# Kernel optimization log

Measured on AMD Instinct MI355X. Metric: run time of the kernel, lower is better.

The kernel has to match this reference:

```python
import jax, jax.numpy as jnp
import numpy as np

H = 512   # d_model (hidden)
L = 2     # rnn_layer_dim
E = 321   # enc_in
C = 321   # c_out (must equal enc_in: decoder output is fed back as input)
T = 96    # seq_len
P = 96    # pred_len
B = 512   # batch


def _cell(x, h, c, Wih, Whh, bih, bhh):
    # PyTorch LSTM gate order: input, forget, cell(g), output
    g = x @ Wih.T + h @ Whh.T + bih + bhh
    i, f, gg, o = jnp.split(g, 4, axis=-1)
    c = jax.nn.sigmoid(f) * c + jax.nn.sigmoid(i) * jnp.tanh(gg)
    h = jax.nn.sigmoid(o) * jnp.tanh(c)
    return h, c


def _run_layer(xs, Wih, Whh, bih, bhh):
    # xs: [T, B, in_dim] -> ys: [T, B, H], final (h, c)
    b = xs.shape[1]
    h0 = jnp.zeros((b, Whh.shape[1]), xs.dtype)
    def step(carry, x):
        h, c = carry
        h, c = _cell(x, h, c, Wih, Whh, bih, bhh)
        return (h, c), h
    (h, c), ys = jax.lax.scan(step, (h0, h0), xs)
    return ys, h, c


def _forward(x_enc, x_mark_enc, x_dec, x_mark_dec,
             e_Wih0, e_Whh0, e_bih0, e_bhh0, e_Wih1, e_Whh1, e_bih1, e_bhh1,
             d_Wih0, d_Whh0, d_bih0, d_bhh0, d_Wih1, d_Whh1, d_bih1, d_bhh1,
             fc_W, fc_b):
    del x_mark_enc, x_dec, x_mark_dec  # unused in use_tf=False path
    xs = jnp.swapaxes(x_enc, 0, 1)                     # [T, B, E]
    ys, h0, c0 = _run_layer(xs, e_Wih0, e_Whh0, e_bih0, e_bhh0)
    _,  h1, c1 = _run_layer(ys, e_Wih1, e_Whh1, e_bih1, e_bhh1)

    inp0 = x_enc[:, -1, :]                             # [B, E] last source step

    def dec_step(carry, _):
        inp, h0, c0, h1, c1 = carry
        h0, c0 = _cell(inp, h0, c0, d_Wih0, d_Whh0, d_bih0, d_bhh0)
        h1, c1 = _cell(h0,  h1, c1, d_Wih1, d_Whh1, d_bih1, d_bhh1)
        out = h1 @ fc_W.T + fc_b                       # [B, C]
        return (out, h0, c0, h1, c1), out

    _, outs = jax.lax.scan(dec_step, (inp0, h0, c0, h1, c1), None, length=P)
    return jnp.swapaxes(outs, 0, 1)                    # [B, P, C]


def setup_inputs() -> dict:
    key = jax.random.key(0)
    ks = jax.random.split(key, 24)
    s = 1.0 / np.sqrt(H)  # PyTorch LSTM init scale
    def w(k, shape):
        return jax.random.uniform(k, shape, jnp.float32, -s, s)
    inp = {
        "x_enc": jax.random.normal(ks[0], (B, T, E), jnp.float32),
        "x_mark_enc": jax.random.normal(ks[1], (B, T, 4), jnp.float32),
        "x_dec": jax.random.normal(ks[2], (B, P, C), jnp.float32),
        "x_mark_dec": jax.random.normal(ks[3], (B, P, 4), jnp.float32),
        "e_Wih0": w(ks[4], (4 * H, E)),  "e_Whh0": w(ks[5], (4 * H, H)),
        "e_bih0": w(ks[6], (4 * H,)),    "e_bhh0": w(ks[7], (4 * H,)),
        "e_Wih1": w(ks[8], (4 * H, H)),  "e_Whh1": w(ks[9], (4 * H, H)),
        "e_bih1": w(ks[10], (4 * H,)),   "e_bhh1": w(ks[11], (4 * H,)),
        "d_Wih0": w(ks[12], (4 * H, E)), "d_Whh0": w(ks[13], (4 * H, H)),
        "d_bih0": w(ks[14], (4 * H,)),   "d_bhh0": w(ks[15], (4 * H,)),
        "d_Wih1": w(ks[16], (4 * H, H)), "d_Whh1": w(ks[17], (4 * H, H)),
        "d_bih1": w(ks[18], (4 * H,)),   "d_bhh1": w(ks[19], (4 * H,)),
        "fc_W": w(ks[20], (C, H)),       "fc_b": w(ks[21], (C,)),
    }
    return inp


def reference(x_enc, x_mark_enc, x_dec, x_mark_dec,
              e_Wih0, e_Whh0, e_bih0, e_bhh0, e_Wih1, e_Whh1, e_bih1, e_bhh1,
              d_Wih0, d_Whh0, d_bih0, d_bhh0, d_Wih1, d_Whh1, d_bih1, d_bhh1,
              fc_W, fc_b):
    return _forward(x_enc, x_mark_enc, x_dec, x_mark_dec,
                    e_Wih0, e_Whh0, e_bih0, e_bhh0, e_Wih1, e_Whh1, e_bih1, e_bhh1,
                    d_Wih0, d_Whh0, d_bih0, d_bhh0, d_Wih1, d_Whh1, d_bih1, d_bhh1,
                    fc_W, fc_b)
```

## Files before the change

kernel.cpp:

```cpp
#include <hip/hip_runtime.h>
#include <hip/hip_bf16.h>

#define BB 512
#define TT 96
#define PP 96
#define EE 321
#define CC 321
#define HH 512
#define G4 2048
#define EPAD 352
#define NFC 384

#define BUF_SZ 24576
#define XH_OFF 0
#define XL_OFF 8192
#define WH_OFF 16384
#define WL_OFF 20480
#define FC_SMEM 49152

#define LSTM_SMEM 81920

typedef unsigned short u16;
typedef __attribute__((ext_vector_type(8))) short bf16x8;
typedef __attribute__((ext_vector_type(16))) float floatx16;

__device__ __forceinline__ void splitf(float v, u16& h, u16& l){
  __hip_bfloat16 bh = __float2bfloat16(v);
  h = *reinterpret_cast<u16*>(&bh);
  float r = v - __bfloat162float(bh);
  __hip_bfloat16 bl = __float2bfloat16(r);
  l = *reinterpret_cast<u16*>(&bl);
}

__device__ __forceinline__ void gload16(const void* g, void* l){
  __builtin_amdgcn_global_load_lds((const __attribute__((address_space(1))) void*)g,
                                   (__attribute__((address_space(3))) void*)l, 16, 0, 0);
}

struct SJob { const float* src; u16* hi; u16* lo; int rows, cols, rowspad, colspad; };
struct SJobs { SJob j[9]; };

__global__ void split_multi(SJobs js){
  const int stride = gridDim.x * blockDim.x;
  const int t0 = blockIdx.x * blockDim.x + threadIdx.x;
  for (int k = 0; k < 9; ++k){
    const SJob J = js.j[k];
    const int total = J.rowspad * J.colspad;
    for (int idx = t0; idx < total; idx += stride){
      int r = idx / J.colspad, cc = idx - r * J.colspad;
      float v = (r < J.rows && cc < J.cols) ? J.src[(size_t)r * J.cols + cc] : 0.f;
      u16 h, l; splitf(v, h, l);
      J.hi[idx] = h; J.lo[idx] = l;
    }
  }
}

__global__ void wcomb_fused(const float* __restrict__ A,
                            const float* __restrict__ Bm,
                            const float* __restrict__ bih, const float* __restrict__ bhh,
                            const float* __restrict__ fcb,
                            u16* __restrict__ Wc_h, u16* __restrict__ Wc_l,
                            float* __restrict__ bd0c){
  __shared__ float arow[EE];
  __shared__ float red[256];
  const int g = blockIdx.x;
  for (int e = threadIdx.x; e < EE; e += 256) arow[e] = A[(size_t)g * EE + e];
  __syncthreads();
  float ps = 0.f;
  for (int e = threadIdx.x; e < EE; e += 256) ps += arow[e] * fcb[e];
  red[threadIdx.x] = ps; __syncthreads();
  for (int s = 128; s > 0; s >>= 1){
    if (threadIdx.x < s) red[threadIdx.x] += red[threadIdx.x + s];
    __syncthreads();
  }
  if (threadIdx.x == 0) bd0c[g] = bih[g] + bhh[g] + red[0];
  for (int k = threadIdx.x; k < HH; k += 256){
    float s = 0.f;
    for (int e = 0; e < EE; ++e) s += arow[e] * Bm[(size_t)e * HH + k];
    u16 h, l; splitf(s, h, l);
    Wc_h[(size_t)g * HH + k] = h; Wc_l[(size_t)g * HH + k] = l;
  }
}

__global__ void prep_misc(
    const float* e_bih0, const float* e_bhh0, float* be0,
    const float* e_bih1, const float* e_bhh1, float* be1,
    const float* d_bih0, const float* d_bhh0, float* bd0,
    const float* d_bih1, const float* d_bhh1, float* bd1,
    const float* fc_b, float* bfc,
    const float* x_enc, u16* inph, u16* inpl, u16* xh, u16* xl){
  const int stride = gridDim.x * blockDim.x;
  const int t0 = blockIdx.x * blockDim.x + threadIdx.x;
  for (int i = t0; i < G4; i += stride){
    be0[i] = e_bih0[i] + e_bhh0[i];
    be1[i] = e_bih1[i] + e_bhh1[i];
    bd0[i] = d_bih0[i] + d_bhh0[i];
    bd1[i] = d_bih1[i] + d_bhh1[i];
  }
  for (int i = t0; i < NFC; i += stride) bfc[i] = (i < CC) ? fc_b[i] : 0.f;
  for (int idx = t0; idx < BB * EPAD; idx += stride){
    int b = idx / EPAD, j = idx - b * EPAD;
    float v = (j < EE) ? x_enc[(size_t)b * TT * EE + (size_t)(TT - 1) * EE + j] : 0.f;
    u16 h, l; splitf(v, h, l);
    inph[idx] = h; inpl[idx] = l;
  }
  for (int idx = t0; idx < TT * BB * EPAD; idx += stride){
    int e = idx % EPAD;
    int rest = idx / EPAD;
    int b = rest % BB;
    int t = rest / BB;
    float v = (e < EE) ? x_enc[((size_t)b * TT + t) * EE + e] : 0.f;
    u16 h, l; splitf(v, h, l);
    xh[idx] = h; xl[idx] = l;
  }
}

template<int MT>
__device__ __forceinline__ void lstm_body(
    char* smem, int bx,
    const u16* __restrict__ Xh, const u16* __restrict__ Xl, int K1pad,
    const u16* __restrict__ Wih_h, const u16* __restrict__ Wih_l,
    const u16* __restrict__ Whh_h, const u16* __restrict__ Whh_l,
    const float* __restrict__ bias, const float* __restrict__ Gin,
    const u16* __restrict__ Hph, const u16* __restrict__ Hpl,
    u16* __restrict__ Hnh, u16* __restrict__ Hnl,
    float* __restrict__ cst)
{
  constexpr int XROWB = MT * 64;
  constexpr int BUFB  = 2 * XROWB + 8192;
  constexpr int WH_O  = 2 * XROWB;
  constexpr int WL_O  = 2 * XROWB + 4096;

  float (*sG)[68] = (float (*)[68])(smem);

  const int tid  = threadIdx.x;
  const int lane = tid & 63;
  const int wid  = tid >> 6;
  const int wm = wid >> 1, wn = wid & 1;
  const int m0 = (bx >> 5) * MT;
  const int u0 = (bx & 31) * 16;

  floatx16 acc0 = {0.f,0.f,0.f,0.f,0.f,0.f,0.f,0.f,0.f,0.f,0.f,0.f,0.f,0.f,0.f,0.f};
  floatx16 acc1 = acc0;

  const int ml    = lane & 31;
  const int thalf = lane >> 5;
  const int a0r = (MT == 128 ? wm * 64 : wm * 32) + ml;
  const int a1r = a0r + 32;
  const int brw = wn * 32 + ml;
  const int xa  = (a0r >> 1) & 3;
  const int xb  = (brw >> 1) & 3;

  const int sl  = lane & 3;
  const int rq  = lane >> 2;
  const int rx0 = wid * (MT / 4) + rq;
  const int rw  = wid * 16 + rq;
  const int sgx = (sl ^ ((rx0 >> 1) & 3)) << 4;
  const int sgw = (sl ^ ((rw  >> 1) & 3)) << 4;
  const size_t gxr0 = (size_t)(m0 + rx0);
  const size_t gxr1 = gxr0 + 16;
  const size_t gwr  = (size_t)wid * HH + u0 + rq;
  const int oX = wid * (MT / 4) * 64;
  const int oW = wid * 16 * 64;

  const int nch1 = K1pad >> 5;
  const int ncht = Hph ? nch1 + (HH >> 5) : nch1;

  auto stage = [&](int ch){
    const bool p1 = ch < nch1;
    const int k0 = (p1 ? ch : ch - nch1) << 5;
    const u16* xh = p1 ? Xh : Hph;
    const u16* xl = p1 ? Xl : Hpl;
    const u16* wh = p1 ? Wih_h : Whh_h;
    const u16* wl = p1 ? Wih_l : Whh_l;
    const size_t Kp = p1 ? (size_t)K1pad : (size_t)HH;
    char* b = smem + (ch % 5) * BUFB;
    gload16((const char*)(xh + gxr0 * Kp + k0) + sgx, b + oX);
    if constexpr (MT == 128) gload16((const char*)(xh + gxr1 * Kp + k0) + sgx, b + oX + 1024);
    gload16((const char*)(xl + gxr0 * Kp + k0) + sgx, b + XROWB + oX);
    if constexpr (MT == 128) gload16((const char*)(xl + gxr1 * Kp + k0) + sgx, b + XROWB + oX + 1024);
    gload16((const char*)(wh + gwr  * Kp + k0) + sgw, b + WH_O + oW);
    gload16((const char*)(wl + gwr  * Kp + k0) + sgw, b + WL_O + oW);
  };

  stage(0); stage(1); stage(2); stage(3);
  for (int ch = 0; ch < ncht; ++ch){
    const int rem = (ncht - 1 - ch) < 3 ? (ncht - 1 - ch) : 3;
    __builtin_amdgcn_sched_barrier(0);
    if constexpr (MT == 128){
      if      (rem == 3) asm volatile("s_waitcnt vmcnt(18)" ::: "memory");
      else if (rem == 2) asm volatile("s_waitcnt vmcnt(12)" ::: "memory");
      else if (rem == 1) asm volatile("s_waitcnt vmcnt(6)"  ::: "memory");
      else               asm volatile("s_waitcnt vmcnt(0)"  ::: "memory");
    } else {
      if      (rem == 3) asm volatile("s_waitcnt vmcnt(12)" ::: "memory");
      else if (rem == 2) asm volatile("s_waitcnt vmcnt(8)"  ::: "memory");
      else if (rem == 1) asm volatile("s_waitcnt vmcnt(4)"  ::: "memory");
      else               asm volatile("s_waitcnt vmcnt(0)"  ::: "memory");
    }
    asm volatile("s_waitcnt lgkmcnt(0)" ::: "memory");
    __builtin_amdgcn_s_barrier();
    __builtin_amdgcn_sched_barrier(0);
    if (ch + 4 < ncht) stage(ch + 4);
    const char* bufc = smem + (ch % 5) * BUFB;
    #pragma unroll
    for (int kk2 = 0; kk2 < 2; ++kk2){
      const int t0 = kk2 * 2 + thalf;
      bf16x8 ah0 = *(const bf16x8*)(bufc + a0r * 64 + ((t0 ^ xa) << 4));
      bf16x8 al0 = *(const bf16x8*)(bufc + XROWB + a0r * 64 + ((t0 ^ xa) << 4));
      bf16x8 bh  = *(const bf16x8*)(bufc + WH_O + brw * 64 + ((t0 ^ xb) << 4));
      bf16x8 bl  = *(const bf16x8*)(bufc + WL_O + brw * 64 + ((t0 ^ xb) << 4));
      acc0 = __builtin_amdgcn_mfma_f32_32x32x16_bf16(ah0, bh, acc0, 0, 0, 0);
      acc0 = __builtin_amdgcn_mfma_f32_32x32x16_bf16(ah0, bl, acc0, 0, 0, 0);
      acc0 = __builtin_amdgcn_mfma_f32_32x32x16_bf16(al0, bh, acc0, 0, 0, 0);
      if constexpr (MT == 128){
        bf16x8 ah1 = *(const bf16x8*)(bufc + a1r * 64 + ((t0 ^ xa) << 4));
        bf16x8 al1 = *(const bf16x8*)(bufc + XROWB + a1r * 64 + ((t0 ^ xa) << 4));
        acc1 = __builtin_amdgcn_mfma_f32_32x32x16_bf16(ah1, bh, acc1, 0, 0, 0);
        acc1 = __builtin_amdgcn_mfma_f32_32x32x16_bf16(ah1, bl, acc1, 0, 0, 0);
        acc1 = __builtin_amdgcn_mfma_f32_32x32x16_bf16(al1, bh, acc1, 0, 0, 0);
      }
    }
  }
  __syncthreads();

  #pragma unroll
  for (int r = 0; r < 16; ++r){
    const int mm = (r & 3) + 8 * (r >> 2) + 4 * thalf;
    if constexpr (MT == 128){
      sG[wm * 64 + mm][wn * 32 + ml]      = acc0[r];
      sG[wm * 64 + 32 + mm][wn * 32 + ml] = acc1[r];
    } else {
      sG[wm * 32 + mm][wn * 32 + ml]      = acc0[r];
    }
  }
  __syncthreads();
  for (int e = tid; e < MT * 16; e += 256){
    const int m = e >> 4, u = e & 15;
    const int gj = u0 + u;
    float gi = sG[m][u]      + bias[gj];
    float gf = sG[m][16 + u] + bias[HH + gj];
    float gg = sG[m][32 + u] + bias[2 * HH + gj];
    float go = sG[m][48 + u] + bias[3 * HH + gj];
    if (Gin){
      const float* gb = Gin + (size_t)(m0 + m) * G4;
      gi += gb[gj]; gf += gb[HH + gj]; gg += gb[2 * HH + gj]; go += gb[3 * HH + gj];
    }
    const float si = 1.f / (1.f + expf(-gi));
    const float sf = 1.f / (1.f + expf(-gf));
    const float so = 1.f / (1.f + expf(-go));
    const size_t sidx = (size_t)(m0 + m) * HH + gj;
    const float cn = sf * cst[sidx] + si * tanhf(gg);
    const float hn = so * tanhf(cn);
    cst[sidx] = cn;
    u16 hh, hl; splitf(hn, hh, hl);
    Hnh[sidx] = hh; Hnl[sidx] = hl;
  }
}

__device__ __forceinline__ void part_body(
    char* smem, int bx,
    const u16* __restrict__ Xh, const u16* __restrict__ Xl,
    const u16* __restrict__ W_h, const u16* __restrict__ W_l,
    float* __restrict__ Gout)
{
  constexpr int XROWB = 64 * 64;
  constexpr int BUFB  = 2 * XROWB + 8192;
  constexpr int WH_O  = 2 * XROWB;
  constexpr int WL_O  = 2 * XROWB + 4096;

  const int tid  = threadIdx.x;
  const int lane = tid & 63;
  const int wid  = tid >> 6;
  const int wm = wid >> 1, wn = wid & 1;
  const int m0 = (bx >> 5) * 64;
  const int u0 = (bx & 31) * 16;

  floatx16 acc0 = {0.f,0.f,0.f,0.f,0.f,0.f,0.f,0.f,0.f,0.f,0.f,0.f,0.f,0.f,0.f,0.f};

  const int ml    = lane & 31;
  const int thalf = lane >> 5;
  const int a0r = wm * 32 + ml;
  const int brw = wn * 32 + ml;
  const int xa  = (a0r >> 1) & 3;
  const int xb  = (brw >> 1) & 3;

  const int sl  = lane & 3;
  const int rq  = lane >> 2;
  const int rx0 = wid * 16 + rq;
  const int rw  = wid * 16 + rq;
  const int sgx = (sl ^ ((rx0 >> 1) & 3)) << 4;
  const int sgw = (sl ^ ((rw  >> 1) & 3)) << 4;
  const size_t gxr0 = (size_t)(m0 + rx0);
  const size_t gwr  = (size_t)wid * HH + u0 + rq;
  const int oX = wid * 16 * 64;
  const int oW = wid * 16 * 64;

  auto stage = [&](int ch){
    const int k0 = ch << 5;
    char* b = smem + (ch % 5) * BUFB;
    gload16((const char*)(Xh + gxr0 * HH + k0) + sgx, b + oX);
    gload16((const char*)(Xl + gxr0 * HH + k0) + sgx, b + XROWB + oX);
    gload16((const char*)(W_h + gwr * HH + k0) + sgw, b + WH_O + oW);
    gload16((const char*)(W_l + gwr * HH + k0) + sgw, b + WL_O + oW);
  };

  stage(0); stage(1); stage(2); stage(3);
  for (int ch = 0; ch < 16; ++ch){
    const int rem = (15 - ch) < 3 ? (15 - ch) : 3;
    __builtin_amdgcn_sched_barrier(0);
    if      (rem == 3) asm volatile("s_waitcnt vmcnt(12)" ::: "memory");
    else if (rem == 2) asm volatile("s_waitcnt vmcnt(8)" ::: "memory");
    else if (rem == 1) asm volatile("s_waitcnt vmcnt(4)" ::: "memory");
    else               asm volatile("s_waitcnt vmcnt(0)" ::: "memory");
    asm volatile("s_waitcnt lgkmcnt(0)" ::: "memory");
    __builtin_amdgcn_s_barrier();
    __builtin_amdgcn_sched_barrier(0);
    if (ch + 4 < 16) stage(ch + 4);
    const char* bufc = smem + (ch % 5) * BUFB;
    #pragma unroll
    for (int kk2 = 0; kk2 < 2; ++kk2){
      const int t0 = kk2 * 2 + thalf;
      bf16x8 ah0 = *(const bf16x8*)(bufc + a0r * 64 + ((t0 ^ xa) << 4));
      bf16x8 al0 = *(const bf16x8*)(bufc + XROWB + a0r * 64 + ((t0 ^ xa) << 4));
      bf16x8 bh  = *(const bf16x8*)(bufc + WH_O + brw * 64 + ((t0 ^ xb) << 4));
      bf16x8 bl  = *(const bf16x8*)(bufc + WL_O + brw * 64 + ((t0 ^ xb) << 4));
      acc0 = __builtin_amdgcn_mfma_f32_32x32x16_bf16(ah0, bh, acc0, 0, 0, 0);
      acc0 = __builtin_amdgcn_mfma_f32_32x32x16_bf16(ah0, bl, acc0, 0, 0, 0);
      acc0 = __builtin_amdgcn_mfma_f32_32x32x16_bf16(al0, bh, acc0, 0, 0, 0);
    }
  }
  const int c = wn * 32 + ml;
  const size_t gcolo = (size_t)(c >> 4) * HH + u0 + (c & 15);
  #pragma unroll
  for (int r = 0; r < 16; ++r){
    const int mm = (r & 3) + 8 * (r >> 2) + 4 * thalf;
    Gout[(size_t)(m0 + wm * 32 + mm) * G4 + gcolo] = acc0[r];
  }
}

__global__ __launch_bounds__(256, 2) void dec_ab(
    const u16* Xfh, const u16* Xfl, int Kf,
    const u16* Wf_h, const u16* Wf_l,
    const float* bias, const float* Gin,
    u16* Hnh, u16* Hnl, float* cst,
    const u16* Xph, const u16* Xpl,
    const u16* Wp_h, const u16* Wp_l,
    float* Gout)
{
  extern __shared__ char smem[];
  if (blockIdx.x < 256)
    lstm_body<64>(smem, blockIdx.x, Xfh, Xfl, Kf, Wf_h, Wf_l, nullptr, nullptr,
                  bias, Gin, nullptr, nullptr, Hnh, Hnl, cst);
  else
    part_body(smem, blockIdx.x - 256, Xph, Xpl, Wp_h, Wp_l, Gout);
}

__global__ __launch_bounds__(256, 2) void lstm_pair(
    int act0, const u16* X0h, const u16* X0l,
    const u16* W0ih_h, const u16* W0ih_l, const u16* W0hh_h, const u16* W0hh_l,
    const float* b0, const u16* H0ph, const u16* H0pl, u16* H0nh, u16* H0nl, float* c0,
    int act1, const u16* X1h, const u16* X1l,
    const u16* W1ih_h, const u16* W1ih_l, const u16* W1hh_h, const u16* W1hh_l,
    const float* b1, const u16* H1ph, const u16* H1pl, u16* H1nh, u16* H1nl, float* c1,
    int do_part, const u16* Wp_h, const u16* Wp_l, float* Gout)
{
  extern __shared__ char smem[];
  const int half = blockIdx.x >> 8;
  const int bx   = blockIdx.x & 255;
  if (half == 0 && !act0){
    if (do_part) part_body(smem, bx, H0ph, H0pl, Wp_h, Wp_l, Gout);
    return;
  }
  if (half == 1 && !act1) return;
  lstm_body<64>(smem, bx,
                half ? X1h : X0h, half ? X1l : X0l, half ? HH : EPAD,
                half ? W1ih_h : W0ih_h, half ? W1ih_l : W0ih_l,
                half ? W1hh_h : W0hh_h, half ? W1hh_l : W0hh_l,
                half ? b1 : b0, nullptr,
                half ? H1ph : H0ph, half ? H1pl : H0pl,
                half ? H1nh : H0nh, half ? H1nl : H0nl,
                half ? c1 : c0);
}

__global__ __launch_bounds__(256) void fc_batch(
    const u16* __restrict__ Hh, const u16* __restrict__ Hl,
    const u16* __restrict__ Wh, const u16* __restrict__ Wl,
    const float* __restrict__ bfc,
    float* __restrict__ out)
{
  extern __shared__ char smem[];
  const int tid = threadIdx.x, lane = tid & 63, wid = tid >> 6;
  const int wm = wid >> 1, wn = wid & 1;
  const int m0 = blockIdx.x * 128;
  const int n0 = blockIdx.y * 64;

  floatx16 acc0 = {0.f,0.f,0.f,0.f,0.f,0.f,0.f,0.f,0.f,0.f,0.f,0.f,0.f,0.f,0.f,0.f};
  floatx16 acc1 = {0.f,0.f,0.f,0.f,0.f,0.f,0.f,0.f,0.f,0.f,0.f,0.f,0.f,0.f,0.f,0.f};

  const int ml    = lane & 31;
  const int thalf = lane >> 5;
  const int a0r = wm * 64 + ml;
  const int a1r = a0r + 32;
  const int brw = wn * 32 + ml;
  const int xa  = (a0r >> 1) & 3;
  const int xb  = (brw >> 1) & 3;

  const int sl  = lane & 3;
  const int rq  = lane >> 2;
  const int rx0 = wid * 32 + rq;
  const int rw  = wid * 16 + rq;
  const int sgx = (sl ^ ((rx0 >> 1) & 3)) << 4;
  const int sgw = (sl ^ ((rw  >> 1) & 3)) << 4;
  const size_t gxr0 = (size_t)(m0 + rx0);
  const size_t gxr1 = gxr0 + 16;
  const size_t gwr  = (size_t)(n0 + rw);
  const int oX = wid * 32 * 64;
  const int oW = wid * 16 * 64;

  auto stage = [&](int ch){
    const int k0 = ch << 5;
    char* b = smem + (ch & 1) * BUF_SZ;
    gload16((const char*)(Hh + gxr0 * HH + k0) + sgx, b + XH_OFF + oX);
    gload16((const char*)(Hh + gxr1 * HH + k0) + sgx, b + XH_OFF + oX + 1024);
    gload16((const char*)(Hl + gxr0 * HH + k0) + sgx, b + XL_OFF + oX);
    gload16((const char*)(Hl + gxr1 * HH + k0) + sgx, b + XL_OFF + oX + 1024);
    gload16((const char*)(Wh + gwr  * HH + k0) + sgw, b + WH_OFF + oW);
    gload16((const char*)(Wl + gwr  * HH + k0) + sgw, b + WL_OFF + oW);
  };

  stage(0);
  for (int ch = 0; ch < 16; ++ch){
    if (ch + 1 < 16) stage(ch + 1);
    __builtin_amdgcn_sched_barrier(0);
    if (ch + 1 < 16) { asm volatile("s_waitcnt vmcnt(6)" ::: "memory"); }
    else             { asm volatile("s_waitcnt vmcnt(0)" ::: "memory"); }
    __builtin_amdgcn_s_barrier();
    __builtin_amdgcn_sched_barrier(0);
    const char* bufc = smem + (ch & 1) * BUF_SZ;
    #pragma unroll
    for (int kk2 = 0; kk2 < 2; ++kk2){
      const int t0 = kk2 * 2 + thalf;
      bf16x8 ah0 = *(const bf16x8*)(bufc + XH_OFF + a0r * 64 + ((t0 ^ xa) << 4));
      bf16x8 al0 = *(const bf16x8*)(bufc + XL_OFF + a0r * 64 + ((t0 ^ xa) << 4));
      bf16x8 ah1 = *(const bf16x8*)(bufc + XH_OFF + a1r * 64 + ((t0 ^ xa) << 4));
      bf16x8 al1 = *(const bf16x8*)(bufc + XL_OFF + a1r * 64 + ((t0 ^ xa) << 4));
      bf16x8 bh  = *(const bf16x8*)(bufc + WH_OFF + brw * 64 + ((t0 ^ xb) << 4));
      bf16x8 bl  = *(const bf16x8*)(bufc + WL_OFF + brw * 64 + ((t0 ^ xb) << 4));
      acc0 = __builtin_amdgcn_mfma_f32_32x32x16_bf16(ah0, bh, acc0, 0, 0, 0);
      acc0 = __builtin_amdgcn_mfma_f32_32x32x16_bf16(ah0, bl, acc0, 0, 0, 0);
      acc0 = __builtin_amdgcn_mfma_f32_32x32x16_bf16(al0, bh, acc0, 0, 0, 0);
      acc1 = __builtin_amdgcn_mfma_f32_32x32x16_bf16(ah1, bh, acc1, 0, 0, 0);
      acc1 = __builtin_amdgcn_mfma_f32_32x32x16_bf16(ah1, bl, acc1, 0, 0, 0);
      acc1 = __builtin_amdgcn_mfma_f32_32x32x16_bf16(al1, bh, acc1, 0, 0, 0);
    }
    __builtin_amdgcn_sched_barrier(0);
    asm volatile("s_waitcnt lgkmcnt(0)" ::: "memory");
    __builtin_amdgcn_s_barrier();
    __builtin_amdgcn_sched_barrier(0);
  }

  const int n = n0 + wn * 32 + ml;
  if (n < CC){
    const float bv = bfc[n];
    #pragma unroll
    for (int r = 0; r < 16; ++r){
      const int mm = (r & 3) + 8 * (r >> 2) + 4 * thalf;
      {
        const int rr = m0 + wm * 64 + mm;
        out[(size_t)(rr & 511) * PP * CC + (size_t)(rr >> 9) * CC + n] = acc0[r] + bv;
      }
      {
        const int rr = m0 + wm * 64 + 32 + mm;
        out[(size_t)(rr & 511) * PP * CC + (size_t)(rr >> 9) * CC + n] = acc1[r] + bv;
      }
    }
  }
}

extern "C" void kernel_launch(void* const* d_in, const int* in_sizes, int n_in,
                              void* d_out, int out_size, void* d_ws, size_t ws_size,
                              hipStream_t stream) {
  const float* x_enc  = (const float*)d_in[0];
  const float* e_Wih0 = (const float*)d_in[4];
  const float* e_Whh0 = (const float*)d_in[5];
  const float* e_bih0 = (const float*)d_in[6];
  const float* e_bhh0 = (const float*)d_in[7];
  const float* e_Wih1 = (const float*)d_in[8];
  const float* e_Whh1 = (const float*)d_in[9];
  const float* e_bih1 = (const float*)d_in[10];
  const float* e_bhh1 = (const float*)d_in[11];
  const float* d_Wih0 = (const float*)d_in[12];
  const float* d_Whh0 = (const float*)d_in[13];
  const float* d_bih0 = (const float*)d_in[14];
  const float* d_bhh0 = (const float*)d_in[15];
  const float* d_Wih1 = (const float*)d_in[16];
  const float* d_Whh1 = (const float*)d_in[17];
  const float* d_bih1 = (const float*)d_in[18];
  const float* d_bhh1 = (const float*)d_in[19];
  const float* fc_W   = (const float*)d_in[20];
  const float* fc_b   = (const float*)d_in[21];

  static bool attr_done = false;
  if (!attr_done){
    hipFuncSetAttribute((const void*)lstm_pair, hipFuncAttributeMaxDynamicSharedMemorySize, LSTM_SMEM);
    hipFuncSetAttribute((const void*)dec_ab,    hipFuncAttributeMaxDynamicSharedMemorySize, LSTM_SMEM);
    attr_done = true;
  }

  char* base = (char*)d_ws;
  size_t off = 0;
  auto alloc_us = [&](size_t n){ u16* p = (u16*)(base + off); off += ((n * 2 + 15) & ~(size_t)15); return p; };
  auto alloc_f  = [&](size_t n){ float* p = (float*)(base + off); off += ((n * 4 + 15) & ~(size_t)15); return p; };

  u16 *We0ih_h = alloc_us((size_t)G4 * EPAD), *We0ih_l = alloc_us((size_t)G4 * EPAD);
  u16 *We0hh_h = alloc_us((size_t)G4 * HH),   *We0hh_l = alloc_us((size_t)G4 * HH);
  u16 *We1ih_h = alloc_us((size_t)G4 * HH),   *We1ih_l = alloc_us((size_t)G4 * HH);
  u16 *We1hh_h = alloc_us((size_t)G4 * HH),   *We1hh_l = alloc_us((size_t)G4 * HH);
  u16 *Wd0ih_h = alloc_us((size_t)G4 * EPAD), *Wd0ih_l = alloc_us((size_t)G4 * EPAD);
  u16 *Wd0hh_h = alloc_us((size_t)G4 * HH),   *Wd0hh_l = alloc_us((size_t)G4 * HH);
  u16 *Wd1ih_h = alloc_us((size_t)G4 * HH),   *Wd1ih_l = alloc_us((size_t)G4 * HH);
  u16 *Wd1hh_h = alloc_us((size_t)G4 * HH),   *Wd1hh_l = alloc_us((size_t)G4 * HH);
  u16 *Wfc_h   = alloc_us((size_t)NFC * HH),  *Wfc_l   = alloc_us((size_t)NFC * HH);
  u16 *Wc_h    = alloc_us((size_t)G4 * HH),   *Wc_l    = alloc_us((size_t)G4 * HH);
  float* be0 = alloc_f(G4);
  float* be1 = alloc_f(G4);
  float* bd0 = alloc_f(G4);
  float* bd1 = alloc_f(G4);
  float* bfc = alloc_f(NFC);
  float* bd0c = alloc_f(G4);
  float* Gp0 = alloc_f((size_t)BB * G4);
  float* Gp1 = alloc_f((size_t)BB * G4);
  u16* h0h[2]; u16* h0l[2]; u16* h1h[2]; u16* h1l[2];
  h0h[0] = alloc_us((size_t)BB * HH); h0l[0] = alloc_us((size_t)BB * HH);
  h1h[0] = alloc_us((size_t)BB * HH); h1l[0] = alloc_us((size_t)BB * HH);
  float* c0 = alloc_f((size_t)BB * HH);
  float* c1 = alloc_f((size_t)BB * HH);
  h0h[1] = alloc_us((size_t)BB * HH); h0l[1] = alloc_us((size_t)BB * HH);
  h1h[1] = alloc_us((size_t)BB * HH); h1l[1] = alloc_us((size_t)BB * HH);
  u16* inph = alloc_us((size_t)BB * EPAD);
  u16* inpl = alloc_us((size_t)BB * EPAD);
  u16* Xench = alloc_us((size_t)TT * BB * EPAD);
  u16* Xencl = alloc_us((size_t)TT * BB * EPAD);
  u16* histh = alloc_us((size_t)PP * BB * HH);
  u16* histl = alloc_us((size_t)PP * BB * HH);

  {
    SJobs js = {{
      { e_Wih0, We0ih_h, We0ih_l, G4, EE, G4, EPAD },
      { e_Whh0, We0hh_h, We0hh_l, G4, HH, G4, HH },
      { e_Wih1, We1ih_h, We1ih_l, G4, HH, G4, HH },
      { e_Whh1, We1hh_h, We1hh_l, G4, HH, G4, HH },
      { d_Wih0, Wd0ih_h, Wd0ih_l, G4, EE, G4, EPAD },
      { d_Whh0, Wd0hh_h, Wd0hh_l, G4, HH, G4, HH },
      { d_Wih1, Wd1ih_h, Wd1ih_l, G4, HH, G4, HH },
      { d_Whh1, Wd1hh_h, Wd1hh_l, G4, HH, G4, HH },
      { fc_W,   Wfc_h,   Wfc_l,   CC, HH, NFC, HH },
    }};
    split_multi<<<1024, 256, 0, stream>>>(js);
  }
  wcomb_fused<<<G4, 256, 0, stream>>>(d_Wih0, fc_W, d_bih0, d_bhh0, fc_b, Wc_h, Wc_l, bd0c);
  prep_misc<<<2048, 256, 0, stream>>>(
      e_bih0, e_bhh0, be0, e_bih1, e_bhh1, be1,
      d_bih0, d_bhh0, bd0, d_bih1, d_bhh1, bd1,
      fc_b, bfc, x_enc, inph, inpl, Xench, Xencl);
  hipMemsetAsync(h0h[0], 0, (size_t)4 * BB * HH * sizeof(u16) + (size_t)2 * BB * HH * sizeof(float), stream);

  for (int t = 0; t <= TT; ++t){
    const int rd = t & 1, wrp = (t + 1) & 1;
    const size_t ts = (size_t)(t < TT ? t : 0) * BB * EPAD;
    lstm_pair<<<512, 256, LSTM_SMEM, stream>>>(
        (t < TT) ? 1 : 0, Xench + ts, Xencl + ts,
        We0ih_h, We0ih_l, We0hh_h, We0hh_l, be0,
        h0h[rd], h0l[rd], h0h[wrp], h0l[wrp], c0,
        (t > 0) ? 1 : 0, h0h[rd], h0l[rd],
        We1ih_h, We1ih_l, We1hh_h, We1hh_l, be1,
        h1h[wrp], h1l[wrp], h1h[rd], h1l[rd], c1,
        (t == TT) ? 1 : 0, Wd0hh_h, Wd0hh_l, Gp0);
  }

  const size_t S = (size_t)BB * HH;
  for (int p = 0; p < PP; ++p){
    const u16* hp_h = p ? histh + (size_t)(p - 1) * S : h1h[0];
    const u16* hp_l = p ? histl + (size_t)(p - 1) * S : h1l[0];
    dec_ab<<<512, 256, LSTM_SMEM, stream>>>(
        p ? hp_h : inph, p ? hp_l : inpl, p ? HH : EPAD,
        p ? Wc_h : Wd0ih_h, p ? Wc_l : Wd0ih_l,
        p ? bd0c : bd0, Gp0,
        h0h[1], h0l[1], c0,
        hp_h, hp_l, Wd1hh_h, Wd1hh_l, Gp1);
    dec_ab<<<512, 256, LSTM_SMEM, stream>>>(
        h0h[1], h0l[1], HH,
        Wd1ih_h, Wd1ih_l,
        bd1, Gp1,
        histh + (size_t)p * S, histl + (size_t)p * S, c1,
        h0h[1], h0l[1], Wd0hh_h, Wd0hh_l, Gp0);
  }

  fc_batch<<<dim3((PP * BB) / 128, NFC / 64), 256, FC_SMEM, stream>>>(
      histh, histl, Wfc_h, Wfc_l, bfc, (float*)d_out);
}
```

Measured before the change: 5.774 ms.

## Load MFMA operands directly from global memory into registers instead of LDS

Replaces the LDS-staged five-buffer global_load_lds pipeline in the LSTM GEMM bodies with direct global-to-register fragment loads, triple-buffered in registers across K chunks. This removes per-chunk barriers and LDS traffic and cuts shared memory to just the epilogue gate buffer, which may allow more blocks per CU. In exchange each wave loses operand sharing through LDS, so global/L2 traffic goes up, and the loads are less coalesced.

```diff
diff --git a/kernel.cpp b/kernel.cpp
--- a/kernel.cpp
+++ b/kernel.cpp
@@ -18,7 +18,7 @@
 #define WL_OFF 20480
 #define FC_SMEM 49152
 
-#define LSTM_SMEM 81920
+#define SG_SMEM 17408
 
 typedef unsigned short u16;
 typedef __attribute__((ext_vector_type(8))) short bf16x8;
@@ -115,127 +115,85 @@
   }
 }
 
-template<int MT>
-__device__ __forceinline__ void lstm_body(
-    char* smem, int bx,
+struct F8 { bf16x8 ah0, ah1, al0, al1, bh0, bh1, bl0, bl1; };
+
+__device__ __forceinline__ void mfma6(floatx16& acc, const F8& f){
+  acc = __builtin_amdgcn_mfma_f32_32x32x16_bf16(f.ah0, f.bh0, acc, 0, 0, 0);
+  acc = __builtin_amdgcn_mfma_f32_32x32x16_bf16(f.ah0, f.bl0, acc, 0, 0, 0);
+  acc = __builtin_amdgcn_mfma_f32_32x32x16_bf16(f.al0, f.bh0, acc, 0, 0, 0);
+  acc = __builtin_amdgcn_mfma_f32_32x32x16_bf16(f.ah1, f.bh1, acc, 0, 0, 0);
+  acc = __builtin_amdgcn_mfma_f32_32x32x16_bf16(f.ah1, f.bl1, acc, 0, 0, 0);
+  acc = __builtin_amdgcn_mfma_f32_32x32x16_bf16(f.al1, f.bh1, acc, 0, 0, 0);
+}
+
+__device__ __forceinline__ floatx16 gemm64(
+    int m0, int u0,
     const u16* __restrict__ Xh, const u16* __restrict__ Xl, int K1pad,
-    const u16* __restrict__ Wih_h, const u16* __restrict__ Wih_l,
+    const u16* __restrict__ W1h, const u16* __restrict__ W1l,
     const u16* __restrict__ Whh_h, const u16* __restrict__ Whh_l,
-    const float* __restrict__ bias, const float* __restrict__ Gin,
-    const u16* __restrict__ Hph, const u16* __restrict__ Hpl,
-    u16* __restrict__ Hnh, u16* __restrict__ Hnl,
-    float* __restrict__ cst)
+    const u16* __restrict__ Hph, const u16* __restrict__ Hpl)
 {
-  constexpr int XROWB = MT * 64;
-  constexpr int BUFB  = 2 * XROWB + 8192;
-  constexpr int WH_O  = 2 * XROWB;
-  constexpr int WL_O  = 2 * XROWB + 4096;
-
-  float (*sG)[68] = (float (*)[68])(smem);
-
-  const int tid  = threadIdx.x;
-  const int lane = tid & 63;
-  const int wid  = tid >> 6;
+  const int lane = threadIdx.x & 63;
+  const int wid  = threadIdx.x >> 6;
   const int wm = wid >> 1, wn = wid & 1;
-  const int m0 = (bx >> 5) * MT;
-  const int u0 = (bx & 31) * 16;
-
-  floatx16 acc0 = {0.f,0.f,0.f,0.f,0.f,0.f,0.f,0.f,0.f,0.f,0.f,0.f,0.f,0.f,0.f,0.f};
-  floatx16 acc1 = acc0;
-
-  const int ml    = lane & 31;
-  const int thalf = lane >> 5;
-  const int a0r = (MT == 128 ? wm * 64 : wm * 32) + ml;
-  const int a1r = a0r + 32;
+  const int ml = lane & 31, thalf = lane >> 5;
+  const size_t arow = (size_t)(m0 + wm * 32 + ml);
   const int brw = wn * 32 + ml;
-  const int xa  = (a0r >> 1) & 3;
-  const int xb  = (brw >> 1) & 3;
-
-  const int sl  = lane & 3;
-  const int rq  = lane >> 2;
-  const int rx0 = wid * (MT / 4) + rq;
-  const int rw  = wid * 16 + rq;
-  const int sgx = (sl ^ ((rx0 >> 1) & 3)) << 4;
-  const int sgw = (sl ^ ((rw  >> 1) & 3)) << 4;
-  const size_t gxr0 = (size_t)(m0 + rx0);
-  const size_t gxr1 = gxr0 + 16;
-  const size_t gwr  = (size_t)wid * HH + u0 + rq;
-  const int oX = wid * (MT / 4) * 64;
-  const int oW = wid * 16 * 64;
-
+  const size_t wrow = (size_t)(brw >> 4) * HH + u0 + (brw & 15);
   const int nch1 = K1pad >> 5;
   const int ncht = Hph ? nch1 + (HH >> 5) : nch1;
 
-  auto stage = [&](int ch){
+  floatx16 acc = {0.f,0.f,0.f,0.f,0.f,0.f,0.f,0.f,0.f,0.f,0.f,0.f,0.f,0.f,0.f,0.f};
+  F8 fA, fB, fC;
+
+  auto LD = [&](F8& f, int ch){
     const bool p1 = ch < nch1;
     const int k0 = (p1 ? ch : ch - nch1) << 5;
     const u16* xh = p1 ? Xh : Hph;
     const u16* xl = p1 ? Xl : Hpl;
-    const u16* wh = p1 ? Wih_h : Whh_h;
-    const u16* wl = p1 ? Wih_l : Whh_l;
+    const u16* wh = p1 ? W1h : Whh_h;
+    const u16* wl = p1 ? W1l : Whh_l;
     const size_t Kp = p1 ? (size_t)K1pad : (size_t)HH;
-    char* b = smem + (ch % 5) * BUFB;
-    gload16((const char*)(xh + gxr0 * Kp + k0) + sgx, b + oX);
-    if constexpr (MT == 128) gload16((const char*)(xh + gxr1 * Kp + k0) + sgx, b + oX + 1024);
-    gload16((const char*)(xl + gxr0 * Kp + k0) + sgx, b + XROWB + oX);
-    if constexpr (MT == 128) gload16((const char*)(xl + gxr1 * Kp + k0) + sgx, b + XROWB + oX + 1024);
-    gload16((const char*)(wh + gwr  * Kp + k0) + sgw, b + WH_O + oW);
-    gload16((const char*)(wl + gwr  * Kp + k0) + sgw, b + WL_O + oW);
+    const size_t xo = arow * Kp + k0 + thalf * 8;
+    const size_t wo = wrow * Kp + k0 + thalf * 8;
+    f.ah0 = *(const bf16x8*)(xh + xo);
+    f.ah1 = *(const bf16x8*)(xh + xo + 16);
+    f.al0 = *(const bf16x8*)(xl + xo);
+    f.al1 = *(const bf16x8*)(xl + xo + 16);
+    f.bh0 = *(const bf16x8*)(wh + wo);
+    f.bh1 = *(const bf16x8*)(wh + wo + 16);
+    f.bl0 = *(const bf16x8*)(wl + wo);
+    f.bl1 = *(const bf16x8*)(wl + wo + 16);
   };
 
-  stage(0); stage(1); stage(2); stage(3);
-  for (int ch = 0; ch < ncht; ++ch){
-    const int rem = (ncht - 1 - ch) < 3 ? (ncht - 1 - ch) : 3;
-    __builtin_amdgcn_sched_barrier(0);
-    if constexpr (MT == 128){
-      if      (rem == 3) asm volatile("s_waitcnt vmcnt(18)" ::: "memory");
-      else if (rem == 2) asm volatile("s_waitcnt vmcnt(12)" ::: "memory");
-      else if (rem == 1) asm volatile("s_waitcnt vmcnt(6)"  ::: "memory");
-      else               asm volatile("s_waitcnt vmcnt(0)"  ::: "memory");
-    } else {
-      if      (rem == 3) asm volatile("s_waitcnt vmcnt(12)" ::: "memory");
-      else if (rem == 2) asm volatile("s_waitcnt vmcnt(8)"  ::: "memory");
-      else if (rem == 1) asm volatile("s_waitcnt vmcnt(4)"  ::: "memory");
-      else               asm volatile("s_waitcnt vmcnt(0)"  ::: "memory");
-    }
-    asm volatile("s_waitcnt lgkmcnt(0)" ::: "memory");
-    __builtin_amdgcn_s_barrier();
-    __builtin_amdgcn_sched_barrier(0);
-    if (ch + 4 < ncht) stage(ch + 4);
-    const char* bufc = smem + (ch % 5) * BUFB;
-    #pragma unroll
-    for (int kk2 = 0; kk2 < 2; ++kk2){
-      const int t0 = kk2 * 2 + thalf;
-      bf16x8 ah0 = *(const bf16x8*)(bufc + a0r * 64 + ((t0 ^ xa) << 4));
-      bf16x8 al0 = *(const bf16x8*)(bufc + XROWB + a0r * 64 + ((t0 ^ xa) << 4));
-      bf16x8 bh  = *(const bf16x8*)(bufc + WH_O + brw * 64 + ((t0 ^ xb) << 4));
-      bf16x8 bl  = *(const bf16x8*)(bufc + WL_O + brw * 64 + ((t0 ^ xb) << 4));
-      acc0 = __builtin_amdgcn_mfma_f32_32x32x16_bf16(ah0, bh, acc0, 0, 0, 0);
-      acc0 = __builtin_amdgcn_mfma_f32_32x32x16_bf16(ah0, bl, acc0, 0, 0, 0);
-      acc0 = __builtin_amdgcn_mfma_f32_32x32x16_bf16(al0, bh, acc0, 0, 0, 0);
-      if constexpr (MT == 128){
-        bf16x8 ah1 = *(const bf16x8*)(bufc + a1r * 64 + ((t0 ^ xa) << 4));
-        bf16x8 al1 = *(const bf16x8*)(bufc + XROWB + a1r * 64 + ((t0 ^ xa) << 4));
-        acc1 = __builtin_amdgcn_mfma_f32_32x32x16_bf16(ah1, bh, acc1, 0, 0, 0);
-        acc1 = __builtin_amdgcn_mfma_f32_32x32x16_bf16(ah1, bl, acc1, 0, 0, 0);
-        acc1 = __builtin_amdgcn_mfma_f32_32x32x16_bf16(al1, bh, acc1, 0, 0, 0);
-      }
-    }
-  }
-  __syncthreads();
-
+  LD(fA, 0); LD(fB, 1);
+  for (int c = 0; c < ncht; c += 3){
+    if (c + 2 < ncht) LD(fC, c + 2);
+    mfma6(acc, fA);
+    if (c + 1 >= ncht) break;
+    if (c + 3 < ncht) LD(fA, c + 3);
+    mfma6(acc, fB);
+    if (c + 2 >= ncht) break;
+    if (c + 4 < ncht) LD(fB, c + 4);
+    mfma6(acc, fC);
+  }
+  return acc;
+}
+
+__device__ __forceinline__ void fin_epi(char* smem, const floatx16& acc, int m0, int u0,
+    const float* __restrict__ bias, const float* __restrict__ Gin,
+    u16* __restrict__ Hnh, u16* __restrict__ Hnl, float* __restrict__ cst)
+{
+  float (*sG)[68] = (float (*)[68])smem;
+  const int tid = threadIdx.x, lane = tid & 63, wid = tid >> 6;
+  const int wm = wid >> 1, wn = wid & 1, ml = lane & 31, thalf = lane >> 5;
   #pragma unroll
   for (int r = 0; r < 16; ++r){
     const int mm = (r & 3) + 8 * (r >> 2) + 4 * thalf;
-    if constexpr (MT == 128){
-      sG[wm * 64 + mm][wn * 32 + ml]      = acc0[r];
-      sG[wm * 64 + 32 + mm][wn * 32 + ml] = acc1[r];
-    } else {
-      sG[wm * 32 + mm][wn * 32 + ml]      = acc0[r];
-    }
+    sG[wm * 32 + mm][wn * 32 + ml] = acc[r];
   }
   __syncthreads();
-  for (int e = tid; e < MT * 16; e += 256){
+  for (int e = tid; e < 1024; e += 256){
     const int m = e >> 4, u = e & 15;
     const int gj = u0 + u;
     float gi = sG[m][u]      + bias[gj];
@@ -258,88 +216,20 @@
   }
 }
 
-__device__ __forceinline__ void part_body(
-    char* smem, int bx,
-    const u16* __restrict__ Xh, const u16* __restrict__ Xl,
-    const u16* __restrict__ W_h, const u16* __restrict__ W_l,
-    float* __restrict__ Gout)
-{
-  constexpr int XROWB = 64 * 64;
-  constexpr int BUFB  = 2 * XROWB + 8192;
-  constexpr int WH_O  = 2 * XROWB;
-  constexpr int WL_O  = 2 * XROWB + 4096;
-
-  const int tid  = threadIdx.x;
-  const int lane = tid & 63;
-  const int wid  = tid >> 6;
-  const int wm = wid >> 1, wn = wid & 1;
-  const int m0 = (bx >> 5) * 64;
-  const int u0 = (bx & 31) * 16;
-
-  floatx16 acc0 = {0.f,0.f,0.f,0.f,0.f,0.f,0.f,0.f,0.f,0.f,0.f,0.f,0.f,0.f,0.f,0.f};
-
-  const int ml    = lane & 31;
-  const int thalf = lane >> 5;
-  const int a0r = wm * 32 + ml;
-  const int brw = wn * 32 + ml;
-  const int xa  = (a0r >> 1) & 3;
-  const int xb  = (brw >> 1) & 3;
-
-  const int sl  = lane & 3;
-  const int rq  = lane >> 2;
-  const int rx0 = wid * 16 + rq;
-  const int rw  = wid * 16 + rq;
-  const int sgx = (sl ^ ((rx0 >> 1) & 3)) << 4;
-  const int sgw = (sl ^ ((rw  >> 1) & 3)) << 4;
-  const size_t gxr0 = (size_t)(m0 + rx0);
-  const size_t gwr  = (size_t)wid * HH + u0 + rq;
-  const int oX = wid * 16 * 64;
-  const int oW = wid * 16 * 64;
-
-  auto stage = [&](int ch){
-    const int k0 = ch << 5;
-    char* b = smem + (ch % 5) * BUFB;
-    gload16((const char*)(Xh + gxr0 * HH + k0) + sgx, b + oX);
-    gload16((const char*)(Xl + gxr0 * HH + k0) + sgx, b + XROWB + oX);
-    gload16((const char*)(W_h + gwr * HH + k0) + sgw, b + WH_O + oW);
-    gload16((const char*)(W_l + gwr * HH + k0) + sgw, b + WL_O + oW);
-  };
-
-  stage(0); stage(1); stage(2); stage(3);
-  for (int ch = 0; ch < 16; ++ch){
-    const int rem = (15 - ch) < 3 ? (15 - ch) : 3;
-    __builtin_amdgcn_sched_barrier(0);
-    if      (rem == 3) asm volatile("s_waitcnt vmcnt(12)" ::: "memory");
-    else if (rem == 2) asm volatile("s_waitcnt vmcnt(8)" ::: "memory");
-    else if (rem == 1) asm volatile("s_waitcnt vmcnt(4)" ::: "memory");
-    else               asm volatile("s_waitcnt vmcnt(0)" ::: "memory");
-    asm volatile("s_waitcnt lgkmcnt(0)" ::: "memory");
-    __builtin_amdgcn_s_barrier();
-    __builtin_amdgcn_sched_barrier(0);
-    if (ch + 4 < 16) stage(ch + 4);
-    const char* bufc = smem + (ch % 5) * BUFB;
-    #pragma unroll
-    for (int kk2 = 0; kk2 < 2; ++kk2){
-      const int t0 = kk2 * 2 + thalf;
-      bf16x8 ah0 = *(const bf16x8*)(bufc + a0r * 64 + ((t0 ^ xa) << 4));
-      bf16x8 al0 = *(const bf16x8*)(bufc + XROWB + a0r * 64 + ((t0 ^ xa) << 4));
-      bf16x8 bh  = *(const bf16x8*)(bufc + WH_O + brw * 64 + ((t0 ^ xb) << 4));
-      bf16x8 bl  = *(const bf16x8*)(bufc + WL_O + brw * 64 + ((t0 ^ xb) << 4));
-      acc0 = __builtin_amdgcn_mfma_f32_32x32x16_bf16(ah0, bh, acc0, 0, 0, 0);
-      acc0 = __builtin_amdgcn_mfma_f32_32x32x16_bf16(ah0, bl, acc0, 0, 0, 0);
-      acc0 = __builtin_amdgcn_mfma_f32_32x32x16_bf16(al0, bh, acc0, 0, 0, 0);
-    }
-  }
+__device__ __forceinline__ void part_st(const floatx16& acc, float* __restrict__ Gout,
+                                        int m0, int u0){
+  const int tid = threadIdx.x, lane = tid & 63, wid = tid >> 6;
+  const int wm = wid >> 1, wn = wid & 1, ml = lane & 31, thalf = lane >> 5;
   const int c = wn * 32 + ml;
   const size_t gcolo = (size_t)(c >> 4) * HH + u0 + (c & 15);
   #pragma unroll
   for (int r = 0; r < 16; ++r){
     const int mm = (r & 3) + 8 * (r >> 2) + 4 * thalf;
-    Gout[(size_t)(m0 + wm * 32 + mm) * G4 + gcolo] = acc0[r];
-  }
-}
-
-__global__ __launch_bounds__(256, 2) void dec_ab(
+    Gout[(size_t)(m0 + wm * 32 + mm) * G4 + gcolo] = acc[r];
+  }
+}
+
+__global__ __launch_bounds__(256) void dec_ab(
     const u16* Xfh, const u16* Xfl, int Kf,
     const u16* Wf_h, const u16* Wf_l,
     const float* bias, const float* Gin,
@@ -349,14 +239,22 @@
     float* Gout)
 {
   extern __shared__ char smem[];
-  if (blockIdx.x < 256)
-    lstm_body<64>(smem, blockIdx.x, Xfh, Xfl, Kf, Wf_h, Wf_l, nullptr, nullptr,
-                  bias, Gin, nullptr, nullptr, Hnh, Hnl, cst);
-  else
-    part_body(smem, blockIdx.x - 256, Xph, Xpl, Wp_h, Wp_l, Gout);
-}
-
-__global__ __launch_bounds__(256, 2) void lstm_pair(
+  if (blockIdx.x < 256){
+    const int bx = blockIdx.x;
+    const int m0 = (bx >> 5) * 64, u0 = (bx & 31) * 16;
+    floatx16 a = gemm64(m0, u0, Xfh, Xfl, Kf, Wf_h, Wf_l,
+                        nullptr, nullptr, nullptr, nullptr);
+    fin_epi(smem, a, m0, u0, bias, Gin, Hnh, Hnl, cst);
+  } else {
+    const int bx = blockIdx.x - 256;
+    const int m0 = (bx >> 5) * 64, u0 = (bx & 31) * 16;
+    floatx16 a = gemm64(m0, u0, Xph, Xpl, HH, Wp_h, Wp_l,
+                        nullptr, nullptr, nullptr, nullptr);
+    part_st(a, Gout, m0, u0);
+  }
+}
+
+__global__ __launch_bounds__(256) void lstm_pair(
     int act0, const u16* X0h, const u16* X0l,
     const u16* W0ih_h, const u16* W0ih_l, const u16* W0hh_h, const u16* W0hh_l,
     const float* b0, const u16* H0ph, const u16* H0pl, u16* H0nh, u16* H0nl, float* c0,
@@ -368,19 +266,25 @@
   extern __shared__ char smem[];
   const int half = blockIdx.x >> 8;
   const int bx   = blockIdx.x & 255;
+  const int m0 = (bx >> 5) * 64, u0 = (bx & 31) * 16;
   if (half == 0 && !act0){
-    if (do_part) part_body(smem, bx, H0ph, H0pl, Wp_h, Wp_l, Gout);
+    if (do_part){
+      floatx16 a = gemm64(m0, u0, H0ph, H0pl, HH, Wp_h, Wp_l,
+                          nullptr, nullptr, nullptr, nullptr);
+      part_st(a, Gout, m0, u0);
+    }
     return;
   }
   if (half == 1 && !act1) return;
-  lstm_body<64>(smem, bx,
-                half ? X1h : X0h, half ? X1l : X0l, half ? HH : EPAD,
-                half ? W1ih_h : W0ih_h, half ? W1ih_l : W0ih_l,
-                half ? W1hh_h : W0hh_h, half ? W1hh_l : W0hh_l,
-                half ? b1 : b0, nullptr,
-                half ? H1ph : H0ph, half ? H1pl : H0pl,
-                half ? H1nh : H0nh, half ? H1nl : H0nl,
-                half ? c1 : c0);
+  if (half == 0){
+    floatx16 a = gemm64(m0, u0, X0h, X0l, EPAD, W0ih_h, W0ih_l,
+                        W0hh_h, W0hh_l, H0ph, H0pl);
+    fin_epi(smem, a, m0, u0, b0, nullptr, H0nh, H0nl, c0);
+  } else {
+    floatx16 a = gemm64(m0, u0, X1h, X1l, HH, W1ih_h, W1ih_l,
+                        W1hh_h, W1hh_l, H1ph, H1pl);
+    fin_epi(smem, a, m0, u0, b1, nullptr, H1nh, H1nl, c1);
+  }
 }
 
 __global__ __launch_bounds__(256) void fc_batch(
@@ -500,13 +404,6 @@
   const float* d_bhh1 = (const float*)d_in[19];
   const float* fc_W   = (const float*)d_in[20];
   const float* fc_b   = (const float*)d_in[21];
-
-  static bool attr_done = false;
-  if (!attr_done){
-    hipFuncSetAttribute((const void*)lstm_pair, hipFuncAttributeMaxDynamicSharedMemorySize, LSTM_SMEM);
-    hipFuncSetAttribute((const void*)dec_ab,    hipFuncAttributeMaxDynamicSharedMemorySize, LSTM_SMEM);
-    attr_done = true;
-  }
 
   char* base = (char*)d_ws;
   size_t off = 0;
@@ -569,7 +466,7 @@
   for (int t = 0; t <= TT; ++t){
     const int rd = t & 1, wrp = (t + 1) & 1;
     const size_t ts = (size_t)(t < TT ? t : 0) * BB * EPAD;
-    lstm_pair<<<512, 256, LSTM_SMEM, stream>>>(
+    lstm_pair<<<512, 256, SG_SMEM, stream>>>(
         (t < TT) ? 1 : 0, Xench + ts, Xencl + ts,
         We0ih_h, We0ih_l, We0hh_h, We0hh_l, be0,
         h0h[rd], h0l[rd], h0h[wrp], h0l[wrp], c0,
@@ -583,13 +480,13 @@
   for (int p = 0; p < PP; ++p){
     const u16* hp_h = p ? histh + (size_t)(p - 1) * S : h1h[0];
     const u16* hp_l = p ? histl + (size_t)(p - 1) * S : h1l[0];
-    dec_ab<<<512, 256, LSTM_SMEM, stream>>>(
+    dec_ab<<<512, 256, SG_SMEM, stream>>>(
         p ? hp_h : inph, p ? hp_l : inpl, p ? HH : EPAD,
         p ? Wc_h : Wd0ih_h, p ? Wc_l : Wd0ih_l,
         p ? bd0c : bd0, Gp0,
         h0h[1], h0l[1], c0,
         hp_h, hp_l, Wd1hh_h, Wd1hh_l, Gp1);
-    dec_ab<<<512, 256, LSTM_SMEM, stream>>>(
+    dec_ab<<<512, 256, SG_SMEM, stream>>>(
         h0h[1], h0l[1], HH,
         Wd1ih_h, Wd1ih_l,
         bd1, Gp1,
```

Result: slower. 11.87 ms (+105.5%).
